# Kernel tuning notes

Measured on AMD Instinct MI355X. Metric: run time of the kernel, lower is better.

The kernel has to match this reference:

```python
import jax, jax.numpy as jnp
import numpy as np
import math

B, L, C_IN = 32, 1024, 21
D_MODEL, N_HEADS, D_FF, E_LAYERS = 256, 8, 1024, 3
E = D_MODEL // N_HEADS
MOVING_AVG, FACTOR, NUM_CLASS = 5, 1.0, 3


def setup_inputs() -> dict:
    key = jax.random.key(0)
    ks = jax.random.split(key, 12)
    s = 0.05
    return {
        "x_enc": jax.random.normal(ks[0], (B, L, C_IN), jnp.float32),
        "token_w": jax.random.normal(ks[1], (D_MODEL, C_IN, 3), jnp.float32) * s,
        "qw": jax.random.normal(ks[2], (E_LAYERS, D_MODEL, D_MODEL), jnp.float32) * s,
        "qb": jnp.zeros((E_LAYERS, D_MODEL), jnp.float32),
        "kw": jax.random.normal(ks[3], (E_LAYERS, D_MODEL, D_MODEL), jnp.float32) * s,
        "kb": jnp.zeros((E_LAYERS, D_MODEL), jnp.float32),
        "vw": jax.random.normal(ks[4], (E_LAYERS, D_MODEL, D_MODEL), jnp.float32) * s,
        "vb": jnp.zeros((E_LAYERS, D_MODEL), jnp.float32),
        "ow": jax.random.normal(ks[5], (E_LAYERS, D_MODEL, D_MODEL), jnp.float32) * s,
        "ob": jnp.zeros((E_LAYERS, D_MODEL), jnp.float32),
        "c1w": jax.random.normal(ks[6], (E_LAYERS, D_FF, D_MODEL), jnp.float32) * s,
        "c2w": jax.random.normal(ks[7], (E_LAYERS, D_MODEL, D_FF), jnp.float32) * s,
        "norm_w": jnp.ones((D_MODEL,), jnp.float32),
        "norm_b": jnp.zeros((D_MODEL,), jnp.float32),
        "proj_w": jax.random.normal(ks[8], (NUM_CLASS, D_MODEL * L), jnp.float32) * 0.01,
        "proj_b": jnp.zeros((NUM_CLASS,), jnp.float32),
    }


def moving_mean(x, k):
    # x: (B, L, D); replicate-pad front/end by (k-1)//2 then average (AvgPool1d stride 1)
    p = (k - 1) // 2
    xp = jnp.concatenate([jnp.repeat(x[:, :1], p, 1), x, jnp.repeat(x[:, -1:], p, 1)], axis=1)
    Lx = x.shape[1]
    acc = xp[:, :Lx]
    for i in range(1, k):
        acc = acc + xp[:, i:i + Lx]
    return acc / k


def series_decomp(x, k):
    m = moving_mean(x, k)
    return x - m, m


def autocorrelation(q, k_, v):
    # q,k_,v: (B, L, H, E). Period-based dependency via FFT cross-correlation.
    Lq = q.shape[1]
    qf = jnp.fft.rfft(q.transpose(0, 2, 3, 1), axis=-1)   # (B,H,E,L//2+1)
    kf = jnp.fft.rfft(k_.transpose(0, 2, 3, 1), axis=-1)
    corr = jnp.fft.irfft(qf * jnp.conj(kf), n=Lq, axis=-1)  # (B,H,E,L)
    vals = v.transpose(0, 2, 3, 1)                          # (B,H,E,L)
    top_k = int(FACTOR * math.log(Lq))
    mean_corr = corr.mean(axis=(1, 2))                      # (B,L)
    weights, delay = jax.lax.top_k(mean_corr, top_k)        # (B,k)
    w = jax.nn.softmax(weights, axis=-1)                    # (B,k)
    # rolled gather: pattern[b,h,e,i,l] = vals[b,h,e,(l+delay[b,i]) % L]
    idx = (jnp.arange(Lq)[None, None, :] + delay[:, :, None]) % Lq  # (B,k,L)
    patterns = jax.vmap(lambda vb, ib: vb[:, :, ib])(vals, idx)      # (B,H,E,k,L)
    out = jnp.einsum('bhekl,bk->bhel', patterns, w)
    return out.transpose(0, 3, 1, 2)  # (B,L,H,E)


def encoder_layer(x, qw, qb, kw, kb, vw, vb, ow, ob, c1w, c2w):
    Bx, Lx, _ = x.shape
    q = (x @ qw.T + qb).reshape(Bx, Lx, N_HEADS, E)
    k_ = (x @ kw.T + kb).reshape(Bx, Lx, N_HEADS, E)
    v = (x @ vw.T + vb).reshape(Bx, Lx, N_HEADS, E)
    a = autocorrelation(q, k_, v).reshape(Bx, Lx, D_MODEL)
    a = a @ ow.T + ob
    x, _ = series_decomp(x + a, MOVING_AVG)
    y = jax.nn.gelu(jnp.einsum('bld,fd->blf', x, c1w), approximate=False)  # Conv1d k=1
    y = jnp.einsum('blf,df->bld', y, c2w)
    res, _ = series_decomp(x + y, MOVING_AVG)
    return res


def my_layernorm(x, w, b):
    mu = x.mean(-1, keepdims=True)
    var = ((x - mu) ** 2).mean(-1, keepdims=True)
    xh = (x - mu) / jnp.sqrt(var + 1e-5) * w + b
    return xh - xh.mean(axis=1, keepdims=True)  # subtract seasonal bias over time


def token_embed(x, w):
    # circular-padded Conv1d(C_IN -> D_MODEL, kernel 3, no bias)
    xt = x.transpose(0, 2, 1)                                   # (B,C,L)
    xp = jnp.pad(xt, ((0, 0), (0, 0), (1, 1)), mode='wrap')
    out = jax.lax.conv_general_dilated(xp, w, (1,), 'VALID')     # (B,D,L)
    return out.transpose(0, 2, 1)


def reference(x_enc, token_w, qw, qb, kw, kb, vw, vb, ow, ob, c1w, c2w, norm_w, norm_b, proj_w, proj_b):
    x = token_embed(x_enc, token_w)
    for l in range(E_LAYERS):
        x = encoder_layer(x, qw[l], qb[l], kw[l], kb[l], vw[l], vb[l], ow[l], ob[l], c1w[l], c2w[l])
    x = my_layernorm(x, norm_w, norm_b)
    out = jax.nn.gelu(x, approximate=False)
    out = out.reshape(out.shape[0], -1)  # (B, L*D_MODEL)
    return out @ proj_w.T + proj_b
```

## Files before the change

kernel.cpp:

```cpp
#include <hip/hip_runtime.h>
#include <hip/hip_bf16.h>
#include <math.h>

#define BB 32
#define LL 1024
#define C_IN 21
#define DM 256
#define DFF 1024
#define NLAYERS 3
#define TOPK 6
#define TOPC 16
#define LSCALE 4096.0f
#define LINV (1.0f/4096.0f)

typedef __attribute__((ext_vector_type(8))) short short8v;
typedef __attribute__((ext_vector_type(8))) _Float16 half8;
typedef __attribute__((ext_vector_type(4))) float f32x4;

__device__ __forceinline__ float gelu_f(float v){
    return 0.5f * v * (1.0f + erff(v * 0.7071067811865476f));
}
__device__ __forceinline__ ushort f2h_bits(float f){
    _Float16 h = (_Float16)f;
    return __builtin_bit_cast(ushort, h);
}
__device__ __forceinline__ float h2f(ushort u){
    return (float)__builtin_bit_cast(_Float16, u);
}

__global__ __launch_bounds__(256) void split_w_k(const float* __restrict__ src,
                                                 ushort* __restrict__ h, ushort* __restrict__ l, int n){
    int i = blockIdx.x*256 + threadIdx.x;
    if (i < n){
        float f = src[i];
        _Float16 hh = (_Float16)f;
        h[i] = __builtin_bit_cast(ushort, hh);
        l[i] = f2h_bits((f - (float)hh) * LSCALE);
    }
}
__global__ __launch_bounds__(256) void split_w_strided(const float* __restrict__ src,
                                                       ushort* __restrict__ h, ushort* __restrict__ l,
                                                       int n, int src_ls, int dst_ls, int dst_off){
    int i = blockIdx.x*256 + threadIdx.x;
    if (i < n){
        int layer = i / src_ls, r = i % src_ls;
        float f = src[i];
        _Float16 hh = (_Float16)f;
        size_t d = (size_t)layer*dst_ls + dst_off + r;
        h[d] = __builtin_bit_cast(ushort, hh);
        l[d] = f2h_bits((f - (float)hh) * LSCALE);
    }
}
__global__ __launch_bounds__(256) void cat_bias_k(const float* __restrict__ b1,
                                                  const float* __restrict__ b2,
                                                  float* __restrict__ out, int n){
    int i = blockIdx.x*256 + threadIdx.x;
    if (i < n){
        int layer = i / 512, c = i % 512;
        out[i] = (c < 256) ? b1[layer*256 + c] : b2[layer*256 + c - 256];
    }
}
__global__ __launch_bounds__(256) void transpose_tw(const float* __restrict__ src,
                                                    float* __restrict__ dst){
    int i = blockIdx.x*256 + threadIdx.x;
    if (i < 256*63){
        int d = i / 63, k = i % 63;
        dst[k*256 + d] = src[i];
    }
}

__global__ __launch_bounds__(256) void token_embed_k(const float* __restrict__ x,
                                                     const float* __restrict__ wT,
                                                     float* __restrict__ out){
    int b = blockIdx.x, l0 = blockIdx.y*32;
    int d = threadIdx.x;
    __shared__ float xs[34][C_IN];
    for (int i = threadIdx.x; i < 34*C_IN; i += 256){
        int r = i / C_IN, c = i % C_IN;
        int g = (l0 - 1 + r + LL) & (LL-1);
        xs[r][c] = x[(size_t)b*LL*C_IN + (size_t)g*C_IN + c];
    }
    float w[63];
    #pragma unroll
    for (int k=0;k<63;k++) w[k] = wT[k*256 + d];
    __syncthreads();
    for (int i=0;i<32;i++){
        float acc = 0.f;
        #pragma unroll
        for (int c=0;c<C_IN;c++){
            acc += xs[i][c]   * w[c*3+0];
            acc += xs[i+1][c] * w[c*3+1];
            acc += xs[i+2][c] * w[c*3+2];
        }
        out[((size_t)b*LL + l0+i)*DM + d] = acc;
    }
}

template<int AMODE, bool BIAS, bool GELU, int OMODE, bool ZSPLIT>
__global__ __launch_bounds__(256) void gemm_mfma_split(const void* __restrict__ Av,
                                                       const void* __restrict__ Av2,
                                                       const ushort* __restrict__ Wh,
                                                       const ushort* __restrict__ Wl,
                                                       const float* __restrict__ bias,
                                                       void* __restrict__ Cv,
                                                       void* __restrict__ C2v,
                                                       void* __restrict__ C3v,
                                                       void* __restrict__ C4v,
                                                       int M, int N, int K){
    __shared__ __align__(16) ushort Ah_s[128*32];
    __shared__ __align__(16) ushort Al_s[128*32];
    __shared__ __align__(16) ushort Wh_s[64*32];
    __shared__ __align__(16) ushort Wl_s[64*32];

    const int tid = threadIdx.x;
    const int MB = M >> 7;
    const int bx = blockIdx.x % MB, by = blockIdx.x / MB;
    const int bm = bx << 7, bn = by << 6;

    const int lane = tid & 63;
    const int wid  = tid >> 6;
    const int wm = wid >> 1, wn = wid & 1;
    const int lr = lane & 15, lg = lane >> 4;

    int aoff[4], boff[2];
    #pragma unroll
    for (int f=0; f<4; f++){
        int ar = wm*64 + f*16 + lr;
        aoff[f] = ar*32 + (lg ^ ((ar>>1)&3))*8;
    }
    #pragma unroll
    for (int g=0; g<2; g++){
        int br = wn*32 + g*16 + lr;
        boff[g] = br*32 + (lg ^ ((br>>1)&3))*8;
    }

    f32x4 acc[4][2], accX[4][2];
    #pragma unroll
    for (int i=0;i<4;i++)
        #pragma unroll
        for (int j=0;j<2;j++){
            acc[i][j]  = (f32x4){0.f,0.f,0.f,0.f};
            accX[i][j] = (f32x4){0.f,0.f,0.f,0.f};
        }

    const int kbeg = ZSPLIT ? (int)blockIdx.y * (K>>1) : 0;
    const int kend = ZSPLIT ? kbeg + (K>>1) : K;

    for (int k0=kbeg; k0<kend; k0+=32){
        #pragma unroll
        for (int i=0;i<2;i++){
            int c = i*256 + tid;
            int row = c >> 2, ko = c & 3;
            int sw = ko ^ ((row>>1)&3);
            int dst = row*32 + sw*8;
            if (AMODE == 2){
                const ushort* Ah_g = (const ushort*)Av;
                const ushort* Al_g = (const ushort*)Av2;
                size_t src = (size_t)(bm+row)*K + k0 + ko*8;
                *reinterpret_cast<short8v*>(&Ah_s[dst]) = *reinterpret_cast<const short8v*>(Ah_g + src);
                *reinterpret_cast<short8v*>(&Al_s[dst]) = *reinterpret_cast<const short8v*>(Al_g + src);
            } else {
                const float* A = (const float*)Av;
                const float* p = A + (size_t)(bm+row)*K + k0 + ko*8;
                float4 f0 = *reinterpret_cast<const float4*>(p);
                float4 f1 = *reinterpret_cast<const float4*>(p+4);
                float vals[8] = {f0.x,f0.y,f0.z,f0.w,f1.x,f1.y,f1.z,f1.w};
                short8v hv, lv;
                #pragma unroll
                for (int j=0;j<8;j++){
                    _Float16 hh = (_Float16)vals[j];
                    hv[j] = (short)__builtin_bit_cast(ushort, hh);
                    lv[j] = (short)f2h_bits((vals[j] - (float)hh) * LSCALE);
                }
                *reinterpret_cast<short8v*>(&Ah_s[dst]) = hv;
                *reinterpret_cast<short8v*>(&Al_s[dst]) = lv;
            }
        }
        {
            int row = tid >> 2, ko = tid & 3;
            int sw = ko ^ ((row>>1)&3);
            int dst = row*32 + sw*8;
            size_t src = (size_t)(bn+row)*K + k0 + ko*8;
            *reinterpret_cast<short8v*>(&Wh_s[dst]) = *reinterpret_cast<const short8v*>(Wh + src);
            *reinterpret_cast<short8v*>(&Wl_s[dst]) = *reinterpret_cast<const short8v*>(Wl + src);
        }
        __syncthreads();

        short8v af[4], al[4], bf_[2], bl[2];
        #pragma unroll
        for (int f=0; f<4; f++){
            af[f] = *reinterpret_cast<short8v*>(&Ah_s[aoff[f]]);
            al[f] = *reinterpret_cast<short8v*>(&Al_s[aoff[f]]);
        }
        #pragma unroll
        for (int g=0; g<2; g++){
            bf_[g] = *reinterpret_cast<short8v*>(&Wh_s[boff[g]]);
            bl[g]  = *reinterpret_cast<short8v*>(&Wl_s[boff[g]]);
        }
        #pragma unroll
        for (int i=0;i<4;i++){
            #pragma unroll
            for (int j=0;j<2;j++){
                acc[i][j] = __builtin_amdgcn_mfma_f32_16x16x32_f16(
                    __builtin_bit_cast(half8, af[i]), __builtin_bit_cast(half8, bf_[j]), acc[i][j], 0,0,0);
                accX[i][j] = __builtin_amdgcn_mfma_f32_16x16x32_f16(
                    __builtin_bit_cast(half8, af[i]), __builtin_bit_cast(half8, bl[j]), accX[i][j], 0,0,0);
                accX[i][j] = __builtin_amdgcn_mfma_f32_16x16x32_f16(
                    __builtin_bit_cast(half8, al[i]), __builtin_bit_cast(half8, bf_[j]), accX[i][j], 0,0,0);
            }
        }
        __syncthreads();
    }

    float* Cout0 = (float*)((ZSPLIT && blockIdx.y) ? C2v : Cv);
    const int crow0 = bm + wm*64, ccol0 = bn + wn*32;
    #pragma unroll
    for (int i=0;i<4;i++){
        #pragma unroll
        for (int j=0;j<2;j++){
            int row0 = crow0 + i*16 + lg*4;
            int col  = ccol0 + j*16 + lr;
            float bv = (BIAS && (!ZSPLIT || blockIdx.y==0)) ? bias[col] : 0.f;
            #pragma unroll
            for (int r=0;r<4;r++){
                float v = acc[i][j][r] + accX[i][j][r]*LINV + bv;
                if (GELU) v = gelu_f(v);
                if (OMODE == 0){
                    Cout0[(size_t)(row0+r)*N + col] = v;
                } else if (OMODE == 2){
                    size_t idx = (size_t)(row0+r)*N + col;
                    _Float16 hh = (_Float16)v;
                    ((ushort*)Cv)[idx]  = __builtin_bit_cast(ushort, hh);
                    ((ushort*)C2v)[idx] = f2h_bits((v - (float)hh) * LSCALE);
                } else {
                    _Float16 hh = (_Float16)v;
                    ushort hb = __builtin_bit_cast(ushort, hh);
                    ushort lb = f2h_bits((v - (float)hh) * LSCALE);
                    if (col < 256){
                        size_t idx = (size_t)(row0+r)*256 + col;
                        ((ushort*)Cv)[idx]  = hb;
                        ((ushort*)C2v)[idx] = lb;
                    } else {
                        size_t idx = (size_t)(row0+r)*256 + (col-256);
                        ((ushort*)C3v)[idx] = hb;
                        ((ushort*)C4v)[idx] = lb;
                    }
                }
            }
        }
    }
}

__global__ __launch_bounds__(256) void corr_mfma(const ushort* __restrict__ qh,
                                                 const ushort* __restrict__ kh,
                                                 float* __restrict__ mc){
    __shared__ __align__(16) ushort Qh_s[128*32];
    __shared__ __align__(16) ushort Kh_s[128*32];
    __shared__ float bins[255];

    const int tid = threadIdx.x;
    int flat = blockIdx.x;
    flat = (flat & 7) * 256 + (flat >> 3);
    const int bxt = flat & 7;
    const int byt = (flat >> 3) & 7;
    const int b   = flat >> 6;
    const int bi = bxt * 128, bj = byt * 128;

    for (int i=tid; i<255; i+=256) bins[i] = 0.f;

    const int lane = tid & 63;
    const int wid  = tid >> 6;
    const int wm = wid >> 1, wn = wid & 1;
    const int lr = lane & 15, lg = lane >> 4;

    int aoff[4], boff[4];
    #pragma unroll
    for (int f=0; f<4; f++){
        int ar = wm*64 + f*16 + lr;
        aoff[f] = ar*32 + (lg ^ ((ar>>1)&3))*8;
        int br = wn*64 + f*16 + lr;
        boff[f] = br*32 + (lg ^ ((br>>1)&3))*8;
    }

    f32x4 acc[4][4];
    #pragma unroll
    for (int i=0;i<4;i++)
        #pragma unroll
        for (int j=0;j<4;j++)
            acc[i][j] = (f32x4){0.f,0.f,0.f,0.f};

    const size_t qbase = (size_t)b*LL*DM;
    const int kbeg = (int)blockIdx.y * (DM>>1);
    const int kend = kbeg + (DM>>1);

    for (int k0=kbeg; k0<kend; k0+=32){
        #pragma unroll
        for (int i=0;i<2;i++){
            int c = i*256 + tid;
            int row = c >> 2, ko = c & 3;
            int sw = ko ^ ((row>>1)&3);
            int dst = row*32 + sw*8;
            *reinterpret_cast<short8v*>(&Qh_s[dst]) =
                *reinterpret_cast<const short8v*>(qh + qbase + (size_t)(bi+row)*DM + k0 + ko*8);
            *reinterpret_cast<short8v*>(&Kh_s[dst]) =
                *reinterpret_cast<const short8v*>(kh + qbase + (size_t)(bj+row)*DM + k0 + ko*8);
        }
        __syncthreads();

        short8v ah[4], bh4[4];
        #pragma unroll
        for (int f=0; f<4; f++){
            ah[f]  = *reinterpret_cast<short8v*>(&Qh_s[aoff[f]]);
            bh4[f] = *reinterpret_cast<short8v*>(&Kh_s[boff[f]]);
        }
        #pragma unroll
        for (int i=0;i<4;i++)
            #pragma unroll
            for (int j=0;j<4;j++)
                acc[i][j] = __builtin_amdgcn_mfma_f32_16x16x32_f16(
                    __builtin_bit_cast(half8, ah[i]), __builtin_bit_cast(half8, bh4[j]), acc[i][j], 0,0,0);
        __syncthreads();
    }

    float pre[7][4];
    #pragma unroll
    for (int d=0; d<7; d++)
        #pragma unroll
        for (int r=0;r<4;r++) pre[d][r]=0.f;
    #pragma unroll
    for (int i=0;i<4;i++)
        #pragma unroll
        for (int j=0;j<4;j++)
            #pragma unroll
            for (int r=0;r<4;r++)
                pre[i-j+3][r] += acc[i][j][r];
    const int bbase = wm*64 - wn*64 + lg*4 - lr + 127;
    #pragma unroll
    for (int d=0; d<7; d++)
        #pragma unroll
        for (int r=0;r<4;r++)
            atomicAdd(&bins[bbase + 16*(d-3) + r], pre[d][r]);
    __syncthreads();
    for (int i=tid; i<255; i+=256){
        int t = ((bi - bj + i - 127) % LL + LL) & (LL-1);
        atomicAdd(&mc[(size_t)b*LL + t], bins[i] * (1.f/256.f));
    }
}

__global__ __launch_bounds__(256) void topcand_kernel(const float* __restrict__ mc,
                                                      int* __restrict__ cand){
    int b = blockIdx.x, tid = threadIdx.x;
    __shared__ float sv[LL];
    __shared__ float rv[256];
    __shared__ int ri[256];
    for (int i=tid;i<LL;i+=256) sv[i] = mc[(size_t)b*LL + i];
    __syncthreads();
    for (int it=0; it<TOPC; it++){
        float best = -1e30f; int bi = LL;
        for (int i=tid;i<LL;i+=256){
            float v = sv[i];
            if (v > best || (v == best && i < bi)){ best = v; bi = i; }
        }
        rv[tid]=best; ri[tid]=bi;
        __syncthreads();
        for (int s=128;s>0;s>>=1){
            if (tid < s){
                if (rv[tid+s] > rv[tid] || (rv[tid+s]==rv[tid] && ri[tid+s]<ri[tid])){
                    rv[tid]=rv[tid+s]; ri[tid]=ri[tid+s];
                }
            }
            __syncthreads();
        }
        if (tid==0){ cand[b*TOPC+it]=ri[0]; sv[ri[0]] = -1e30f; }
        __syncthreads();
    }
}

__global__ __launch_bounds__(256) void rescore_k(const ushort* __restrict__ qh,
                                                 const ushort* __restrict__ ql,
                                                 const ushort* __restrict__ kh,
                                                 const ushort* __restrict__ kl,
                                                 const int* __restrict__ cand,
                                                 float* __restrict__ scores4){
    int i = blockIdx.x;
    int b = (i & 7) | (((i >> 3) & 3) << 3);
    int c = i >> 5;
    int chunk = blockIdx.y;
    int t = cand[b*TOPC + c];
    const size_t base = (size_t)b << 18;
    const int off = t << 8;
    const int mbeg = chunk << 16;
    const int mend = mbeg + (1<<16);
    float s = 0.f, comp = 0.f;
    for (int m = mbeg + threadIdx.x*8; m < mend; m += 256*8){
        int mq = (m + off) & ((1<<18)-1);
        short8v kh8 = *reinterpret_cast<const short8v*>(kh + base + m);
        short8v kl8 = *reinterpret_cast<const short8v*>(kl + base + m);
        short8v qh8 = *reinterpret_cast<const short8v*>(qh + base + mq);
        short8v ql8 = *reinterpret_cast<const short8v*>(ql + base + mq);
        float term = 0.f;
        #pragma unroll
        for (int j=0;j<8;j++){
            float kf = h2f((ushort)kh8[j]) + h2f((ushort)kl8[j])*LINV;
            float qf = h2f((ushort)qh8[j]) + h2f((ushort)ql8[j])*LINV;
            term += kf*qf;
        }
        float y = term - comp;
        float tt = s + y;
        comp = (tt - s) - y;
        s = tt;
    }
    for (int o=32;o>0;o>>=1) s += __shfl_down(s, o, 64);
    __shared__ float red[4];
    if ((threadIdx.x & 63)==0) red[threadIdx.x>>6] = s;
    __syncthreads();
    if (threadIdx.x==0)
        scores4[(size_t)(b*TOPC + c)*4 + chunk] = red[0]+red[1]+red[2]+red[3];
}

__global__ __launch_bounds__(64) void finalize_k(const int* __restrict__ cand,
                                                 const float* __restrict__ scores4,
                                                 int* __restrict__ delays,
                                                 float* __restrict__ wts){
    int b = blockIdx.x;
    int lane = threadIdx.x;
    float v = -1e30f;
    int idx = 1<<30;
    if (lane < TOPC){
        size_t s4 = (size_t)(b*TOPC + lane)*4;
        v = (scores4[s4] + scores4[s4+1] + scores4[s4+2] + scores4[s4+3]) * (1.f/256.f);
        idx = cand[b*TOPC + lane];
    }
    float topv[TOPK]; int topi[TOPK];
    #pragma unroll
    for (int k=0;k<TOPK;k++){
        float bv = v; int bi = idx;
        #pragma unroll
        for (int o=8;o>0;o>>=1){
            float ov = __shfl_xor(bv, o, 16);
            int   oi = __shfl_xor(bi, o, 16);
            if (ov > bv || (ov == bv && oi < bi)){ bv = ov; bi = oi; }
        }
        topv[k]=bv; topi[k]=bi;
        if (idx == bi) v = -1e30f;
    }
    if (lane==0){
        float mx = topv[0];
        float e[TOPK], se=0.f;
        #pragma unroll
        for (int k=0;k<TOPK;k++){ e[k]=expf(topv[k]-mx); se+=e[k]; }
        #pragma unroll
        for (int k=0;k<TOPK;k++){
            wts[b*TOPK+k] = e[k]/se;
            delays[b*TOPK+k] = topi[k];
        }
    }
}

__global__ __launch_bounds__(256) void attn_gather4(const float4* __restrict__ v,
                                                    const int* __restrict__ delays,
                                                    const float* __restrict__ wts,
                                                    float4* __restrict__ a){
    int gid = blockIdx.x*256 + threadIdx.x;
    int d4 = gid & 63;
    int bl = gid >> 6;
    int b = bl >> 10, l = bl & (LL-1);
    const int* dl = delays + b*TOPK;
    const float* w = wts + b*TOPK;
    float ax=0.f, ay=0.f, az=0.f, aw=0.f;
    #pragma unroll
    for (int kk=0;kk<TOPK;kk++){
        int ls = (l + dl[kk]) & (LL-1);
        float4 t = v[(size_t)((b<<10)+ls)*64 + d4];
        float wk = w[kk];
        ax += wk*t.x; ay += wk*t.y; az += wk*t.z; aw += wk*t.w;
    }
    a[gid] = make_float4(ax, ay, az, aw);
}

__global__ __launch_bounds__(256) void add_decomp4(const float4* __restrict__ xa,
                                                   const float4* __restrict__ xb,
                                                   float4* __restrict__ out){
    int d4 = threadIdx.x & 63;
    int rg = threadIdx.x >> 6;
    int b = blockIdx.x;
    int l0 = blockIdx.y*128 + rg*32;
    float4 win[5];
    #pragma unroll
    for (int i=0;i<4;i++){
        int g = l0 - 2 + i;
        g = g < 0 ? 0 : g;
        size_t idx = (size_t)((b<<10) + g)*64 + d4;
        float4 A = xa[idx], Bv = xb[idx];
        win[i] = make_float4(A.x+Bv.x, A.y+Bv.y, A.z+Bv.z, A.w+Bv.w);
    }
    for (int i=0;i<32;i++){
        int g = l0 + 2 + i;
        g = g > LL-1 ? LL-1 : g;
        size_t idx = (size_t)((b<<10) + g)*64 + d4;
        float4 A = xa[idx], Bv = xb[idx];
        win[4] = make_float4(A.x+Bv.x, A.y+Bv.y, A.z+Bv.z, A.w+Bv.w);
        float4 o;
        o.x = win[2].x - (win[0].x+win[1].x+win[2].x+win[3].x+win[4].x)*0.2f;
        o.y = win[2].y - (win[0].y+win[1].y+win[2].y+win[3].y+win[4].y)*0.2f;
        o.z = win[2].z - (win[0].z+win[1].z+win[2].z+win[3].z+win[4].z)*0.2f;
        o.w = win[2].w - (win[0].w+win[1].w+win[2].w+win[3].w+win[4].w)*0.2f;
        out[(size_t)((b<<10) + l0 + i)*64 + d4] = o;
        win[0]=win[1]; win[1]=win[2]; win[2]=win[3]; win[3]=win[4];
    }
}

__global__ __launch_bounds__(256) void add_decomp4_3(const float4* __restrict__ xa,
                                                     const float4* __restrict__ xb,
                                                     const float4* __restrict__ xc,
                                                     float4* __restrict__ out){
    int d4 = threadIdx.x & 63;
    int rg = threadIdx.x >> 6;
    int b = blockIdx.x;
    int l0 = blockIdx.y*128 + rg*32;
    float4 win[5];
    #pragma unroll
    for (int i=0;i<4;i++){
        int g = l0 - 2 + i;
        g = g < 0 ? 0 : g;
        size_t idx = (size_t)((b<<10) + g)*64 + d4;
        float4 A = xa[idx], Bv = xb[idx], Cc = xc[idx];
        win[i] = make_float4(A.x+Bv.x+Cc.x, A.y+Bv.y+Cc.y, A.z+Bv.z+Cc.z, A.w+Bv.w+Cc.w);
    }
    for (int i=0;i<32;i++){
        int g = l0 + 2 + i;
        g = g > LL-1 ? LL-1 : g;
        size_t idx = (size_t)((b<<10) + g)*64 + d4;
        float4 A = xa[idx], Bv = xb[idx], Cc = xc[idx];
        win[4] = make_float4(A.x+Bv.x+Cc.x, A.y+Bv.y+Cc.y, A.z+Bv.z+Cc.z, A.w+Bv.w+Cc.w);
        float4 o;
        o.x = win[2].x - (win[0].x+win[1].x+win[2].x+win[3].x+win[4].x)*0.2f;
        o.y = win[2].y - (win[0].y+win[1].y+win[2].y+win[3].y+win[4].y)*0.2f;
        o.z = win[2].z - (win[0].z+win[1].z+win[2].z+win[3].z+win[4].z)*0.2f;
        o.w = win[2].w - (win[0].w+win[1].w+win[2].w+win[3].w+win[4].w)*0.2f;
        out[(size_t)((b<<10) + l0 + i)*64 + d4] = o;
        win[0]=win[1]; win[1]=win[2]; win[2]=win[3]; win[3]=win[4];
    }
}

__global__ __launch_bounds__(256) void ln_kernel(const float* __restrict__ x,
                                                 const float* __restrict__ nw,
                                                 const float* __restrict__ nb,
                                                 float* __restrict__ xh){
    int bl = blockIdx.x, d = threadIdx.x;
    float val = x[(size_t)bl*DM + d];
    __shared__ float red[4];
    float v = val;
    for (int o=32;o>0;o>>=1) v += __shfl_down(v, o, 64);
    if ((d&63)==0) red[d>>6] = v;
    __syncthreads();
    float mu = (red[0]+red[1]+red[2]+red[3])*(1.f/256.f);
    __syncthreads();
    float diff = val - mu;
    v = diff*diff;
    for (int o=32;o>0;o>>=1) v += __shfl_down(v, o, 64);
    if ((d&63)==0) red[d>>6] = v;
    __syncthreads();
    float var = (red[0]+red[1]+red[2]+red[3])*(1.f/256.f);
    xh[(size_t)bl*DM + d] = diff*rsqrtf(var+1e-5f)*nw[d] + nb[d];
}

__global__ __launch_bounds__(256) void colsum_kernel(const float* __restrict__ xh,
                                                     float* __restrict__ colsum){
    int b = blockIdx.x, chunk = blockIdx.y, d = threadIdx.x;
    float s = 0.f;
    for (int l = chunk*128; l < (chunk+1)*128; l++)
        s += xh[((size_t)b*LL + l)*DM + d];
    atomicAdd(&colsum[b*DM + d], s);
}

__global__ __launch_bounds__(256) void gelu_sub_kernel(const float* __restrict__ xh,
                                                       const float* __restrict__ colsum,
                                                       float* __restrict__ g){
    int bl = blockIdx.x, d = threadIdx.x;
    int b = bl / LL;
    float v = xh[(size_t)bl*DM + d] - colsum[b*DM + d]*(1.f/1024.f);
    g[(size_t)bl*DM + d] = gelu_f(v);
}

__global__ __launch_bounds__(256) void proj_kernel(const float* __restrict__ g,
                                                   const float* __restrict__ pw,
                                                   const float* __restrict__ pb,
                                                   float* __restrict__ out){
    int b = blockIdx.x, c = blockIdx.y, ch = blockIdx.z;
    int tid = threadIdx.x;
    const size_t F = (size_t)LL*DM;
    size_t base = ch*(F/16);
    float s = 0.f;
    for (size_t i = tid; i < F/16; i += 256)
        s += g[(size_t)b*F + base + i] * pw[(size_t)c*F + base + i];
    for (int o=32;o>0;o>>=1) s += __shfl_down(s, o, 64);
    __shared__ float red[4];
    if ((tid&63)==0) red[tid>>6] = s;
    __syncthreads();
    if (tid==0){
        float tot = red[0]+red[1]+red[2]+red[3];
        if (ch==0) tot += pb[c];
        atomicAdd(&out[b*3 + c], tot);
    }
}

extern "C" void kernel_launch(void* const* d_in, const int* in_sizes, int n_in,
                              void* d_out, int out_size, void* d_ws, size_t ws_size,
                              hipStream_t stream) {
    const float* x_enc   = (const float*)d_in[0];
    const float* token_w = (const float*)d_in[1];
    const float* qw = (const float*)d_in[2];
    const float* qb = (const float*)d_in[3];
    const float* kw = (const float*)d_in[4];
    const float* kb = (const float*)d_in[5];
    const float* vw = (const float*)d_in[6];
    const float* vb = (const float*)d_in[7];
    const float* ow = (const float*)d_in[8];
    const float* ob = (const float*)d_in[9];
    const float* c1w = (const float*)d_in[10];
    const float* c2w = (const float*)d_in[11];
    const float* norm_w = (const float*)d_in[12];
    const float* norm_b = (const float*)d_in[13];
    const float* proj_w = (const float*)d_in[14];
    const float* proj_b = (const float*)d_in[15];
    float* outp = (float*)d_out;

    const size_t NTOK = (size_t)BB*LL*DM;
    float* ws = (float*)d_ws;
    float* buf0 = ws;
    float* buf1 = ws + NTOK;
    float* buf2 = ws + 2*NTOK;
    ushort* wu = (ushort*)(ws + 3*NTOK);
    const size_t WSM = (size_t)NLAYERS*DM*DM;
    const size_t WSF = (size_t)NLAYERS*DFF*DM;
    ushort* qkwh = wu;             ushort* qkwl = qkwh + 2*WSM;
    ushort* vwh  = qkwl + 2*WSM;   ushort* vwl  = vwh + WSM;
    ushort* owh  = vwl + WSM;      ushort* owl  = owh + WSM;
    ushort* c1wh = owl + WSM;      ushort* c1wl = c1wh + WSF;
    ushort* c2wh = c1wl + WSF;     ushort* c2wl = c2wh + WSF;
    float* after_w = ws + 3*NTOK + 2359296;
    float* qkbias = after_w;
    float* mc     = qkbias + (size_t)NLAYERS*512;
    float* colsum = mc + (size_t)BB*LL;
    int*   delays = (int*)(colsum + BB*DM);
    float* wts    = (float*)(delays + BB*TOPK);
    int*   cand   = (int*)(wts + BB*TOPK);
    float* scores4 = (float*)(cand + BB*TOPC);
    float* twT    = scores4 + BB*TOPC*4;
    float* buf3   = twT + 63*256;

    const size_t needed_floats = 3*NTOK + 2359296 + (size_t)NLAYERS*512 + (size_t)BB*LL
                               + (size_t)BB*DM + (size_t)BB*TOPK*2 + (size_t)BB*TOPC
                               + (size_t)BB*TOPC*4 + 63*256 + NTOK;
    const bool zs = (ws_size >= needed_floats*sizeof(float));

    hipMemsetAsync(d_out, 0, 96*sizeof(float), stream);

    {
        int n1 = NLAYERS*DM*DM;
        int n2 = NLAYERS*DFF*DM;
        split_w_strided<<<(n1+255)/256, 256, 0, stream>>>(qw, qkwh, qkwl, n1, 65536, 131072, 0);
        split_w_strided<<<(n1+255)/256, 256, 0, stream>>>(kw, qkwh, qkwl, n1, 65536, 131072, 65536);
        cat_bias_k<<<(NLAYERS*512+255)/256, 256, 0, stream>>>(qb, kb, qkbias, NLAYERS*512);
        split_w_k<<<(n1+255)/256, 256, 0, stream>>>(vw, vwh, vwl, n1);
        split_w_k<<<(n1+255)/256, 256, 0, stream>>>(ow, owh, owl, n1);
        split_w_k<<<(n2+255)/256, 256, 0, stream>>>(c1w, c1wh, c1wl, n2);
        split_w_k<<<(n2+255)/256, 256, 0, stream>>>(c2w, c2wh, c2wl, n2);
        transpose_tw<<<(256*63+255)/256, 256, 0, stream>>>(token_w, twT);
    }

    token_embed_k<<<dim3(BB, LL/32), 256, 0, stream>>>(x_enc, twT, buf0);

    const int M = BB*LL;
    const int FFNC = 8192;

    for (int l=0; l<NLAYERS; l++){
        ushort* qkwh_l = qkwh + (size_t)l*512*DM;  ushort* qkwl_l = qkwl + (size_t)l*512*DM;
        ushort* vwh_l = vwh + (size_t)l*DM*DM;     ushort* vwl_l = vwl + (size_t)l*DM*DM;
        ushort* owh_l = owh + (size_t)l*DM*DM;     ushort* owl_l = owl + (size_t)l*DM*DM;
        ushort* c1wh_l = c1wh + (size_t)l*DFF*DM;  ushort* c1wl_l = c1wl + (size_t)l*DFF*DM;
        ushort* c2wh_l = c2wh + (size_t)l*DM*DFF;  ushort* c2wl_l = c2wl + (size_t)l*DM*DFF;
        const float* qkb_l = qkbias + (size_t)l*512;
        const float* vb_l = vb + (size_t)l*DM;
        const float* ob_l = ob + (size_t)l*DM;

        ushort* qh_p = (ushort*)buf1;  ushort* ql_p = qh_p + NTOK;
        ushort* kh_p = (ushort*)buf2;  ushort* kl_p = kh_p + NTOK;
        gemm_mfma_split<0,true,false,3,false><<<(M/128)*(512/64), 256, 0, stream>>>(
            buf0, nullptr, qkwh_l, qkwl_l, qkb_l, qh_p, ql_p, kh_p, kl_p, M, 512, DM);

        hipMemsetAsync(mc, 0, (size_t)BB*LL*sizeof(float), stream);
        corr_mfma<<<dim3(2048, 2), 256, 0, stream>>>(qh_p, kh_p, mc);
        topcand_kernel<<<BB, 256, 0, stream>>>(mc, cand);
        rescore_k<<<dim3(BB*TOPC, 4), 256, 0, stream>>>(qh_p, ql_p, kh_p, kl_p, cand, scores4);
        finalize_k<<<BB, 64, 0, stream>>>(cand, scores4, delays, wts);

        gemm_mfma_split<0,true,false,0,false><<<(M/128)*(DM/64), 256, 0, stream>>>(
            buf0, nullptr, vwh_l, vwl_l, vb_l, buf1, nullptr, nullptr, nullptr, M, DM, DM);
        attn_gather4<<<(BB*LL*64)/256, 256, 0, stream>>>(
            (const float4*)buf1, delays, wts, (float4*)buf2);
        gemm_mfma_split<0,true,false,0,false><<<(M/128)*(DM/64), 256, 0, stream>>>(
            buf2, nullptr, owh_l, owl_l, ob_l, buf1, nullptr, nullptr, nullptr, M, DM, DM);

        add_decomp4<<<dim3(BB, LL/128), 256, 0, stream>>>(
            (const float4*)buf0, (const float4*)buf1, (float4*)buf2);

        ushort* yh_p = (ushort*)buf0;
        ushort* yl_p = yh_p + (size_t)FFNC*DFF;
        for (int c0 = 0; c0 < M; c0 += FFNC){
            gemm_mfma_split<0,false,true,2,false><<<(FFNC/128)*(DFF/64), 256, 0, stream>>>(
                buf2 + (size_t)c0*DM, nullptr, c1wh_l, c1wl_l, nullptr, yh_p, yl_p, nullptr, nullptr, FFNC, DFF, DM);
            if (zs){
                gemm_mfma_split<2,false,false,0,true><<<dim3((FFNC/128)*(DM/64), 2), 256, 0, stream>>>(
                    yh_p, yl_p, c2wh_l, c2wl_l, nullptr,
                    buf1 + (size_t)c0*DM, buf3 + (size_t)c0*DM, nullptr, nullptr, FFNC, DM, DFF);
            } else {
                gemm_mfma_split<2,false,false,0,false><<<(FFNC/128)*(DM/64), 256, 0, stream>>>(
                    yh_p, yl_p, c2wh_l, c2wl_l, nullptr,
                    buf1 + (size_t)c0*DM, nullptr, nullptr, nullptr, FFNC, DM, DFF);
            }
        }

        if (zs)
            add_decomp4_3<<<dim3(BB, LL/128), 256, 0, stream>>>(
                (const float4*)buf2, (const float4*)buf1, (const float4*)buf3, (float4*)buf0);
        else
            add_decomp4<<<dim3(BB, LL/128), 256, 0, stream>>>(
                (const float4*)buf2, (const float4*)buf1, (float4*)buf0);
    }

    ln_kernel<<<BB*LL, 256, 0, stream>>>(buf0, norm_w, norm_b, buf1);
    hipMemsetAsync(colsum, 0, (size_t)BB*DM*sizeof(float), stream);
    colsum_kernel<<<dim3(BB, 8), 256, 0, stream>>>(buf1, colsum);
    gelu_sub_kernel<<<BB*LL, 256, 0, stream>>>(buf1, colsum, buf2);
    proj_kernel<<<dim3(BB, 3, 16), 256, 0, stream>>>(buf2, proj_w, proj_b, outp);
}
```

Before: 2.041 ms.

## Replace global atomics in correlation kernel with scratch slots and reduction kernel

The correlation kernel no longer splits the K dimension across two grid slices. Each block now covers the full depth and writes its 255 diagonal bins to a private scratch slot instead of atomically adding into the per-batch correlation vector. A new reduce kernel sums the overlapping slots for each lag, which removes the memset and the contended global atomics. The cost is an extra launch, a scratch buffer, and half as many blocks, each doing twice the K loop.

Result: faster. 1.840 ms (-9.9%).

```diff
diff --git a/kernel.cpp b/kernel.cpp
--- a/kernel.cpp
+++ b/kernel.cpp
@@ -253,7 +253,7 @@
 
 __global__ __launch_bounds__(256) void corr_mfma(const ushort* __restrict__ qh,
                                                  const ushort* __restrict__ kh,
-                                                 float* __restrict__ mc){
+                                                 float* __restrict__ scr){
     __shared__ __align__(16) ushort Qh_s[128*32];
     __shared__ __align__(16) ushort Kh_s[128*32];
     __shared__ float bins[255];
@@ -290,10 +290,8 @@
             acc[i][j] = (f32x4){0.f,0.f,0.f,0.f};
 
     const size_t qbase = (size_t)b*LL*DM;
-    const int kbeg = (int)blockIdx.y * (DM>>1);
-    const int kend = kbeg + (DM>>1);
-
-    for (int k0=kbeg; k0<kend; k0+=32){
+
+    for (int k0=0; k0<DM; k0+=32){
         #pragma unroll
         for (int i=0;i<2;i++){
             int c = i*256 + tid;
@@ -341,10 +339,25 @@
         for (int r=0;r<4;r++)
             atomicAdd(&bins[bbase + 16*(d-3) + r], pre[d][r]);
     __syncthreads();
-    for (int i=tid; i<255; i+=256){
-        int t = ((bi - bj + i - 127) % LL + LL) & (LL-1);
-        atomicAdd(&mc[(size_t)b*LL + t], bins[i] * (1.f/256.f));
-    }
+    float* slot = scr + ((size_t)(b*64 + byt*8 + bxt) << 8);
+    for (int i=tid; i<255; i+=256) slot[i] = bins[i];
+}
+
+__global__ __launch_bounds__(256) void corr_reduce(const float* __restrict__ scr,
+                                                   float* __restrict__ mc){
+    int b = blockIdx.x;
+    int t = blockIdx.y*256 + threadIdx.x;
+    float s = 0.f;
+    const float* base = scr + ((size_t)b << 14);
+    #pragma unroll
+    for (int byt=0; byt<8; byt++){
+        #pragma unroll
+        for (int bxt=0; bxt<8; bxt++){
+            int i = (t - 128*(bxt - byt) + 127) & (LL-1);
+            if (i < 255) s += base[((byt*8 + bxt) << 8) + i];
+        }
+    }
+    mc[(size_t)b*LL + t] = s * (1.f/256.f);
 }
 
 __global__ __launch_bounds__(256) void topcand_kernel(const float* __restrict__ mc,
@@ -648,11 +661,12 @@
     int*   cand   = (int*)(wts + BB*TOPK);
     float* scores4 = (float*)(cand + BB*TOPC);
     float* twT    = scores4 + BB*TOPC*4;
-    float* buf3   = twT + 63*256;
+    float* scr    = twT + 63*256;
+    float* buf3   = scr + 524288;
 
     const size_t needed_floats = 3*NTOK + 2359296 + (size_t)NLAYERS*512 + (size_t)BB*LL
                                + (size_t)BB*DM + (size_t)BB*TOPK*2 + (size_t)BB*TOPC
-                               + (size_t)BB*TOPC*4 + 63*256 + NTOK;
+                               + (size_t)BB*TOPC*4 + 63*256 + 524288 + NTOK;
     const bool zs = (ws_size >= needed_floats*sizeof(float));
 
     hipMemsetAsync(d_out, 0, 96*sizeof(float), stream);
@@ -690,8 +704,8 @@
         gemm_mfma_split<0,true,false,3,false><<<(M/128)*(512/64), 256, 0, stream>>>(
             buf0, nullptr, qkwh_l, qkwl_l, qkb_l, qh_p, ql_p, kh_p, kl_p, M, 512, DM);
 
-        hipMemsetAsync(mc, 0, (size_t)BB*LL*sizeof(float), stream);
-        corr_mfma<<<dim3(2048, 2), 256, 0, stream>>>(qh_p, kh_p, mc);
+        corr_mfma<<<2048, 256, 0, stream>>>(qh_p, kh_p, scr);
+        corr_reduce<<<dim3(BB, 4), 256, 0, stream>>>(scr, mc);
         topcand_kernel<<<BB, 256, 0, stream>>>(mc, cand);
         rescore_k<<<dim3(BB*TOPC, 4), 256, 0, stream>>>(qh_p, ql_p, kh_p, kl_p, cand, scores4);
         finalize_k<<<BB, 64, 0, stream>>>(cand, scores4, delays, wts);
```
